# Kernel optimization log

Measured on AMD Instinct MI355X. Metric: run time of the kernel, lower is better.

The kernel has to match this reference:

```python
import jax, jax.numpy as jnp
import numpy as np

B, S, D, H = 4, 4096, 256, 4
Dh = D // H


def setup_inputs() -> dict:
    key = jax.random.key(0)
    ks = jax.random.split(key, 5)
    scale = 1.0 / np.sqrt(D)
    return {
        "inputs": jax.random.normal(ks[0], (B, S, D), dtype=jnp.float32),
        "Wq": jax.random.normal(ks[1], (D, D), dtype=jnp.float32) * scale,
        "bq": jnp.zeros((D,), jnp.float32),
        "Wk": jax.random.normal(ks[2], (D, D), dtype=jnp.float32) * scale,
        "bk": jnp.zeros((D,), jnp.float32),
        "Wv": jax.random.normal(ks[3], (D, D), dtype=jnp.float32) * scale,
        "bv": jnp.zeros((D,), jnp.float32),
        "Wo": jax.random.normal(ks[4], (D, D), dtype=jnp.float32) * scale,
        "bo": jnp.zeros((D,), jnp.float32),
    }


def reference(inputs, Wq, bq, Wk, bk, Wv, bv, Wo, bo):
    b, s, d = inputs.shape
    # QKV projections
    q = inputs @ Wq + bq
    k = inputs @ Wk + bk
    v = inputs @ Wv + bv
    # separate heads: [B, S, D] -> [B, H, S, Dh]
    def split_heads(x):
        return x.reshape(b, s, H, Dh).transpose(0, 2, 1, 3)
    q, k, v = split_heads(q), split_heads(k), split_heads(v)
    # scaled dot-product attention (no causal mask: mask=False)
    scores = jnp.einsum("bhqd,bhkd->bhqk", q, k) / jnp.sqrt(jnp.float32(Dh))
    weights = jax.nn.softmax(scores, axis=-1)
    attn = jnp.einsum("bhqk,bhkd->bhqd", weights, v)
    # combine heads: [B, H, S, Dh] -> [B, S, D]
    attn = attn.transpose(0, 2, 1, 3).reshape(b, s, d)
    return attn @ Wo + bo
```

## Files before the change

kernel.cpp:

```cpp
#include <hip/hip_runtime.h>
#include <cmath>

#define B_  4
#define S_  4096
#define D_  256
#define H_  4
#define DH_ 64
#define M_TOTAL (B_*S_)
#define QSCALE 0.1803368801111f

typedef __bf16 bf16x8 __attribute__((ext_vector_type(8)));
typedef __bf16 bf16x4 __attribute__((ext_vector_type(4)));
typedef __bf16 bf16x2 __attribute__((ext_vector_type(2)));
typedef float  f32x4  __attribute__((ext_vector_type(4)));
typedef float  f32x16 __attribute__((ext_vector_type(16)));

#define AS1 __attribute__((address_space(1)))
#define AS3 __attribute__((address_space(3)))

__device__ __forceinline__ void g2lds16(const void* g, void* l) {
    __builtin_amdgcn_global_load_lds((AS1 const void*)g, (AS3 void*)l, 16, 0, 0);
}

#if __has_builtin(__builtin_amdgcn_permlane32_swap)
typedef unsigned uint2v __attribute__((ext_vector_type(2)));
__device__ __forceinline__ void plswap(unsigned &a, unsigned &b) {
    uint2v r = __builtin_amdgcn_permlane32_swap(a, b, false, false);
    a = r[0]; b = r[1];
}
#else
__device__ __forceinline__ void plswap(unsigned &a, unsigned &b) {
    unsigned bl = (unsigned)__shfl_xor((int)b, 32);
    unsigned ah = (unsigned)__shfl_xor((int)a, 32);
    bool hi = (threadIdx.x & 32) != 0;
    unsigned na = hi ? bl : a;
    unsigned nb = hi ? b  : ah;
    a = na; b = nb;
}
#endif

__device__ __forceinline__ unsigned pk2(float x, float y) {
    bf16x2 t; t[0] = (__bf16)x; t[1] = (__bf16)y;
    return __builtin_bit_cast(unsigned, t);
}

__global__ __launch_bounds__(256) void prep(const float* __restrict__ X,
                                            const float* __restrict__ W0,
                                            const float* __restrict__ W1,
                                            const float* __restrict__ W2,
                                            const float* __restrict__ W3,
                                            __bf16* __restrict__ Xb,
                                            __bf16* __restrict__ Wt_all) {
    int t = threadIdx.x;
    if (blockIdx.x < 2048) {
        size_t i = ((size_t)blockIdx.x * 256 + t) * 8;
        float4 v0 = *(const float4*)(X + i);
        float4 v1 = *(const float4*)(X + i + 4);
        bf16x8 o;
        o[0] = (__bf16)v0.x; o[1] = (__bf16)v0.y; o[2] = (__bf16)v0.z; o[3] = (__bf16)v0.w;
        o[4] = (__bf16)v1.x; o[5] = (__bf16)v1.y; o[6] = (__bf16)v1.z; o[7] = (__bf16)v1.w;
        *(bf16x8*)(Xb + i) = o;
        return;
    }
    int bid = blockIdx.x - 2048;
    int z = bid >> 6, rem = bid & 63;
    int by = rem >> 3, bx = rem & 7;
    const float* W = (z == 0) ? W0 : (z == 1) ? W1 : (z == 2) ? W2 : W3;
    float wsc = (z == 0) ? QSCALE : 1.0f;
    __bf16* Wt = Wt_all + (size_t)z * 65536;
    __shared__ float tile[32][33];
    int r0 = by * 32, c0 = bx * 32;
#pragma unroll
    for (int e = 0; e < 4; e++) {
        int idx = t + e * 256; int r = idx >> 5, c = idx & 31;
        tile[r][c] = W[(r0 + r) * 256 + c0 + c];
    }
    __syncthreads();
#pragma unroll
    for (int e = 0; e < 4; e++) {
        int idx = t + e * 256; int r = idx >> 5, c = idx & 31;
        Wt[(c0 + r) * 256 + (r0 + c)] = (__bf16)(tile[c][r] * wsc);
    }
}

__global__ __launch_bounds__(256) void gemm_bt(const __bf16* __restrict__ A,
                                               const __bf16* __restrict__ Wt_all,
                                               const float* __restrict__ bias0,
                                               const float* __restrict__ bias1,
                                               const float* __restrict__ bias2,
                                               __bf16* __restrict__ outb,
                                               __bf16* __restrict__ voutb,
                                               float* __restrict__ outf,
                                               int out_is_f32, float bsc0) {
    constexpr int K = 256;
    __shared__ __attribute__((aligned(16))) __bf16 As[128 * 32];
    __shared__ __attribute__((aligned(16))) __bf16 Bs[128 * 32];

    int t = threadIdx.x;
    int lane = t & 63, w = t >> 6;
    int wr = w >> 1, wc = w & 1;
    int l16 = lane & 15, quad = lane >> 4;
    int mbase = blockIdx.x * 128;
    int nbase = blockIdx.y * 128;
    int z = blockIdx.z;
    const __bf16* Bt = Wt_all + (size_t)z * 65536;
    const float* bias = (z == 0) ? bias0 : (z == 1) ? bias1 : bias2;
    float bscale = (z == 0) ? bsc0 : 1.0f;

    f32x4 acc[4][4] = {};

    int srow = t >> 2;
    int sseg = (t & 3) * 8;

    for (int kk = 0; kk < K; kk += 32) {
        __syncthreads();
        g2lds16(A  + (size_t)(mbase +      srow) * K + kk + sseg, (char*)As +        t * 16);
        g2lds16(A  + (size_t)(mbase + 64 + srow) * K + kk + sseg, (char*)As + 4096 + t * 16);
        g2lds16(Bt + (size_t)(nbase +      srow) * K + kk + sseg, (char*)Bs +        t * 16);
        g2lds16(Bt + (size_t)(nbase + 64 + srow) * K + kk + sseg, (char*)Bs + 4096 + t * 16);
        __syncthreads();

        bf16x8 a[4], b[4];
#pragma unroll
        for (int i = 0; i < 4; i++)
            a[i] = *(const bf16x8*)(As + (wr * 64 + i * 16 + l16) * 32 + quad * 8);
#pragma unroll
        for (int j = 0; j < 4; j++)
            b[j] = *(const bf16x8*)(Bs + (wc * 64 + j * 16 + l16) * 32 + quad * 8);
#pragma unroll
        for (int i = 0; i < 4; i++)
#pragma unroll
            for (int j = 0; j < 4; j++)
                acc[i][j] = __builtin_amdgcn_mfma_f32_16x16x32_bf16(a[i], b[j], acc[i][j], 0, 0, 0);
    }

#pragma unroll
    for (int i = 0; i < 4; i++) {
#pragma unroll
        for (int j = 0; j < 4; j++) {
            int col = nbase + wc * 64 + j * 16 + l16;
            float bv = bias[col] * bscale;
            int row0 = mbase + wr * 64 + i * 16 + quad * 4;
            if (out_is_f32) {
#pragma unroll
                for (int r = 0; r < 4; r++)
                    outf[(size_t)(row0 + r) * 256 + col] = acc[i][j][r] + bv;
            } else if (z == 2) {
                int hcol = col >> 6, dh = col & 63;
                int bidx = row0 >> 12, s0 = row0 & 4095;
                bf16x4 pk;
#pragma unroll
                for (int r = 0; r < 4; r++) pk[r] = (__bf16)(acc[i][j][r] + bv);
                *(bf16x4*)(voutb + ((size_t)(bidx * 4 + hcol) * 64 + dh) * 4096 + s0) = pk;
            } else {
#pragma unroll
                for (int r = 0; r < 4; r++)
                    outb[(size_t)z * ((size_t)M_TOTAL * 256) + (size_t)(row0 + r) * 256 + col] =
                        (__bf16)(acc[i][j][r] + bv);
            }
        }
    }
}

__global__ __launch_bounds__(256, 2) void attn(const __bf16* __restrict__ Qb,
                                               const __bf16* __restrict__ Kb,
                                               const __bf16* __restrict__ Vt,
                                               __bf16* __restrict__ Ctx) {
    __shared__ __attribute__((aligned(16))) __bf16 smem[32768];

    int t = threadIdx.x;
    int lane = t & 63, w = t >> 6;
    int l31 = lane & 31, hh = lane >> 5;

    int lin = blockIdx.x;
    int xcd = lin & 7, j = lin >> 3;
    int bh = xcd * 2 + (j & 1);
    int qblk = j >> 1;
    int b = bh >> 2, hd = bh & 3;
    int qw = qblk * 128 + w * 32;

    const __bf16* Kbase = Kb + (size_t)b * S_ * 256 + hd * 64;
    const __bf16* Vbase = Vt + (size_t)bh * 64 * S_;

    bf16x8 qf[4];
#pragma unroll
    for (int ks = 0; ks < 4; ks++)
        qf[ks] = *(const bf16x8*)(Qb + (size_t)(b * S_ + qw + l31) * 256
                                      + hd * 64 + ks * 16 + hh * 8);

    f32x16 acc[2] = {};
    float lsum = 0.f;

    int srow = t >> 3;
    int sseg = t & 7;

#define STAGE(kv, slot) do {                                                   \
        char* mk = (char*)smem + (slot) * 16384;                               \
        char* mv = mk + 8192;                                                  \
        _Pragma("unroll")                                                      \
        for (int c = 0; c < 2; c++) {                                          \
            int rr = c * 32 + srow;                                            \
            int gseg = (sseg ^ (rr & 7)) * 8;                                  \
            g2lds16(Kbase + (size_t)((kv) + rr) * 256 + gseg,                  \
                    mk + c * 4096 + t * 16);                                   \
            g2lds16(Vbase + (size_t)rr * S_ + (kv) + gseg,                     \
                    mv + c * 4096 + t * 16);                                   \
        }                                                                      \
    } while (0)

    STAGE(0, 0);
    STAGE(64, 1);

    for (int it = 0; it < 64; it++) {
        if (it < 62) {
            STAGE((it + 2) * 64, (it + 2) & 3);
            asm volatile("s_waitcnt vmcnt(8)" ::: "memory");
        } else if (it == 62) {
            asm volatile("s_waitcnt vmcnt(4)" ::: "memory");
        } else {
            asm volatile("s_waitcnt vmcnt(0)" ::: "memory");
        }
        asm volatile("s_barrier" ::: "memory");

        __bf16* Ksp = (__bf16*)((char*)smem + (it & 3) * 16384);
        __bf16* Vsp = Ksp + 4096;

        f32x16 st[2] = {};
#pragma unroll
        for (int kt = 0; kt < 2; kt++) {
            bf16x8 kf[4];
#pragma unroll
            for (int ks = 0; ks < 4; ks++) {
                int slot = (ks * 2 + hh) ^ (l31 & 7);
                kf[ks] = *(const bf16x8*)(Ksp + (kt * 32 + l31) * 64 + slot * 8);
            }
#pragma unroll
            for (int ks = 0; ks < 4; ks++)
                st[kt] = __builtin_amdgcn_mfma_f32_32x32x16_bf16(kf[ks], qf[ks], st[kt], 0, 0, 0);
        }

#pragma unroll
        for (int kt = 0; kt < 2; kt++) {
            float p[16];
#pragma unroll
            for (int r = 0; r < 16; r++) p[r] = __builtin_amdgcn_exp2f(st[kt][r]);
            float s0 = ((p[0] + p[1]) + (p[2] + p[3])) + ((p[4] + p[5]) + (p[6] + p[7]));
            float s1 = ((p[8] + p[9]) + (p[10] + p[11])) + ((p[12] + p[13]) + (p[14] + p[15]));
            lsum += s0 + s1;
            unsigned dd[8];
#pragma unroll
            for (int m = 0; m < 4; m++) {
                dd[m * 2]     = pk2(p[4 * m],     p[4 * m + 1]);
                dd[m * 2 + 1] = pk2(p[4 * m + 2], p[4 * m + 3]);
            }
#pragma unroll
            for (int tt = 0; tt < 2; tt++) {
                int tks = kt * 2 + tt;
                unsigned x0 = dd[4 * tt],     y0 = dd[4 * tt + 2];
                unsigned x1 = dd[4 * tt + 1], y1 = dd[4 * tt + 3];
                plswap(x0, y0);
                plswap(x1, y1);
                union { unsigned u[4]; bf16x8 v; } c;
                c.u[0] = x0; c.u[1] = x1; c.u[2] = y0; c.u[3] = y1;
#pragma unroll
                for (int mt = 0; mt < 2; mt++) {
                    int slot = (tks * 2 + hh) ^ (l31 & 7);
                    bf16x8 vf = *(const bf16x8*)(Vsp + (mt * 32 + l31) * 64 + slot * 8);
                    acc[mt] = __builtin_amdgcn_mfma_f32_32x32x16_bf16(vf, c.v, acc[mt], 0, 0, 0);
                }
            }
        }
    }
#undef STAGE

    float l = lsum;
    l += __shfl_xor(l, 32);
    float inv = 1.f / l;

    __syncthreads();
    __bf16* Es = smem + w * 2304;
#pragma unroll
    for (int mt = 0; mt < 2; mt++) {
#pragma unroll
        for (int rg = 0; rg < 4; rg++) {
            bf16x4 ov;
#pragma unroll
            for (int e = 0; e < 4; e++) ov[e] = (__bf16)(acc[mt][4 * rg + e] * inv);
            int dhb = mt * 32 + rg * 8 + 4 * hh;
            *(bf16x4*)(Es + l31 * 72 + dhb) = ov;
        }
    }
    __syncthreads();
#pragma unroll
    for (int pass = 0; pass < 4; pass++) {
        int q = pass * 8 + (lane >> 3);
        int col = (lane & 7) * 8;
        bf16x8 val = *(const bf16x8*)(Es + q * 72 + col);
        *(bf16x8*)(Ctx + (size_t)(b * S_ + qw + q) * 256 + hd * 64 + col) = val;
    }
}

extern "C" void kernel_launch(void* const* d_in, const int* in_sizes, int n_in,
                              void* d_out, int out_size, void* d_ws, size_t ws_size,
                              hipStream_t stream) {
    const float* X  = (const float*)d_in[0];
    const float* Wq = (const float*)d_in[1];
    const float* bq = (const float*)d_in[2];
    const float* Wk = (const float*)d_in[3];
    const float* bk = (const float*)d_in[4];
    const float* Wv = (const float*)d_in[5];
    const float* bv = (const float*)d_in[6];
    const float* Wo = (const float*)d_in[7];
    const float* bo = (const float*)d_in[8];
    float* out = (float*)d_out;

    char* ws = (char*)d_ws;
    const size_t MB = 1024 * 1024;
    __bf16* Xb  = (__bf16*)(ws);
    __bf16* Ctx = (__bf16*)(ws);
    __bf16* Wt  = (__bf16*)(ws + 8 * MB);
    __bf16* Qb  = (__bf16*)(ws + 8 * MB + 512 * 1024);
    __bf16* Kb  = (__bf16*)((char*)Qb + 8 * MB);
    __bf16* Vt  = (__bf16*)((char*)Kb + 8 * MB);

    prep<<<dim3(2304), dim3(256), 0, stream>>>(X, Wq, Wk, Wv, Wo, Xb, Wt);
    gemm_bt<<<dim3(M_TOTAL / 128, 2, 3), dim3(256), 0, stream>>>(
        Xb, Wt, bq, bk, bv, Qb, Vt, nullptr, 0, QSCALE);
    attn<<<dim3(512), dim3(256), 0, stream>>>(Qb, Kb, Vt, Ctx);
    gemm_bt<<<dim3(M_TOTAL / 128, 2, 1), dim3(256), 0, stream>>>(
        Ctx, Wt + 3 * 65536, bo, bo, bo, nullptr, nullptr, out, 1, 1.0f);
}
```

Measured before the change: 181.6 us.

## Split attention KV tiles across warp pairs and load V directly to registers

```diff
diff --git a/kernel.cpp b/kernel.cpp
--- a/kernel.cpp
+++ b/kernel.cpp
@@ -162,22 +162,23 @@
     }
 }
 
-__global__ __launch_bounds__(256, 2) void attn(const __bf16* __restrict__ Qb,
+__global__ __launch_bounds__(256, 4) void attn(const __bf16* __restrict__ Qb,
                                                const __bf16* __restrict__ Kb,
                                                const __bf16* __restrict__ Vt,
                                                __bf16* __restrict__ Ctx) {
-    __shared__ __attribute__((aligned(16))) __bf16 smem[32768];
+    __shared__ __attribute__((aligned(16))) __bf16 smem[18432];
 
     int t = threadIdx.x;
     int lane = t & 63, w = t >> 6;
     int l31 = lane & 31, hh = lane >> 5;
+    int kw = w & 1, qw2 = w >> 1;
 
     int lin = blockIdx.x;
     int xcd = lin & 7, j = lin >> 3;
     int bh = xcd * 2 + (j & 1);
     int qblk = j >> 1;
     int b = bh >> 2, hd = bh & 3;
-    int qw = qblk * 128 + w * 32;
+    int qw = qblk * 64 + qw2 * 32;
 
     const __bf16* Kbase = Kb + (size_t)b * S_ * 256 + hd * 64;
     const __bf16* Vbase = Vt + (size_t)bh * 64 * S_;
@@ -195,16 +196,13 @@
     int sseg = t & 7;
 
 #define STAGE(kv, slot) do {                                                   \
-        char* mk = (char*)smem + (slot) * 16384;                               \
-        char* mv = mk + 8192;                                                  \
+        char* mk = (char*)smem + (slot) * 8192;                                \
         _Pragma("unroll")                                                      \
         for (int c = 0; c < 2; c++) {                                          \
             int rr = c * 32 + srow;                                            \
             int gseg = (sseg ^ (rr & 7)) * 8;                                  \
             g2lds16(Kbase + (size_t)((kv) + rr) * 256 + gseg,                  \
                     mk + c * 4096 + t * 16);                                   \
-            g2lds16(Vbase + (size_t)rr * S_ + (kv) + gseg,                     \
-                    mv + c * 4096 + t * 16);                                   \
         }                                                                      \
     } while (0)
 
@@ -212,91 +210,109 @@
     STAGE(64, 1);
 
     for (int it = 0; it < 64; it++) {
-        if (it < 62) {
-            STAGE((it + 2) * 64, (it + 2) & 3);
-            asm volatile("s_waitcnt vmcnt(8)" ::: "memory");
-        } else if (it == 62) {
-            asm volatile("s_waitcnt vmcnt(4)" ::: "memory");
-        } else {
-            asm volatile("s_waitcnt vmcnt(0)" ::: "memory");
-        }
+        int kv = it * 64;
+
+        bf16x8 vf[2][2];
+#pragma unroll
+        for (int tt = 0; tt < 2; tt++)
+#pragma unroll
+            for (int mt = 0; mt < 2; mt++)
+                vf[tt][mt] = *(const bf16x8*)(Vbase + (size_t)(mt * 32 + l31) * S_
+                                              + kv + (kw * 2 + tt) * 16 + hh * 8);
+
+        if (it < 62) STAGE(kv + 128, (it + 2) & 3);
+        asm volatile("s_waitcnt vmcnt(8)" ::: "memory");
         asm volatile("s_barrier" ::: "memory");
 
-        __bf16* Ksp = (__bf16*)((char*)smem + (it & 3) * 16384);
-        __bf16* Vsp = Ksp + 4096;
-
-        f32x16 st[2] = {};
-#pragma unroll
-        for (int kt = 0; kt < 2; kt++) {
-            bf16x8 kf[4];
-#pragma unroll
-            for (int ks = 0; ks < 4; ks++) {
-                int slot = (ks * 2 + hh) ^ (l31 & 7);
-                kf[ks] = *(const bf16x8*)(Ksp + (kt * 32 + l31) * 64 + slot * 8);
+        __bf16* Ksp = (__bf16*)((char*)smem + (it & 3) * 8192);
+
+        bf16x8 kf[4];
+#pragma unroll
+        for (int ks = 0; ks < 4; ks++) {
+            int slot = (ks * 2 + hh) ^ (l31 & 7);
+            kf[ks] = *(const bf16x8*)(Ksp + (kw * 32 + l31) * 64 + slot * 8);
+        }
+        f32x16 st = {};
+#pragma unroll
+        for (int ks = 0; ks < 4; ks++)
+            st = __builtin_amdgcn_mfma_f32_32x32x16_bf16(kf[ks], qf[ks], st, 0, 0, 0);
+
+        float p[16];
+#pragma unroll
+        for (int r = 0; r < 16; r++) p[r] = __builtin_amdgcn_exp2f(st[r]);
+        float s0 = ((p[0] + p[1]) + (p[2] + p[3])) + ((p[4] + p[5]) + (p[6] + p[7]));
+        float s1 = ((p[8] + p[9]) + (p[10] + p[11])) + ((p[12] + p[13]) + (p[14] + p[15]));
+        lsum += s0 + s1;
+        unsigned dd[8];
+#pragma unroll
+        for (int m = 0; m < 4; m++) {
+            dd[m * 2]     = pk2(p[4 * m],     p[4 * m + 1]);
+            dd[m * 2 + 1] = pk2(p[4 * m + 2], p[4 * m + 3]);
+        }
+
+#pragma unroll
+        for (int tt = 0; tt < 2; tt++) {
+            unsigned x0 = dd[4 * tt],     y0 = dd[4 * tt + 2];
+            unsigned x1 = dd[4 * tt + 1], y1 = dd[4 * tt + 3];
+            plswap(x0, y0);
+            plswap(x1, y1);
+            union { unsigned u[4]; bf16x8 v; } c;
+            c.u[0] = x0; c.u[1] = x1; c.u[2] = y0; c.u[3] = y1;
+#pragma unroll
+            for (int mt = 0; mt < 2; mt++)
+                acc[mt] = __builtin_amdgcn_mfma_f32_32x32x16_bf16(vf[tt][mt], c.v, acc[mt], 0, 0, 0);
+        }
+    }
+#undef STAGE
+
+    lsum += __shfl_xor(lsum, 32);
+
+    __syncthreads();
+    float* lsd = (float*)((char*)smem + 16384);
+    if (kw == 1) {
+#pragma unroll
+        for (int mt = 0; mt < 2; mt++)
+#pragma unroll
+            for (int g = 0; g < 4; g++) {
+                f32x4 v;
+#pragma unroll
+                for (int e = 0; e < 4; e++) v[e] = acc[mt][4 * g + e];
+                *(f32x4*)((char*)smem + qw2 * 8192 + (mt * 4 + g) * 1024 + lane * 16) = v;
             }
-#pragma unroll
-            for (int ks = 0; ks < 4; ks++)
-                st[kt] = __builtin_amdgcn_mfma_f32_32x32x16_bf16(kf[ks], qf[ks], st[kt], 0, 0, 0);
-        }
-
-#pragma unroll
-        for (int kt = 0; kt < 2; kt++) {
-            float p[16];
-#pragma unroll
-            for (int r = 0; r < 16; r++) p[r] = __builtin_amdgcn_exp2f(st[kt][r]);
-            float s0 = ((p[0] + p[1]) + (p[2] + p[3])) + ((p[4] + p[5]) + (p[6] + p[7]));
-            float s1 = ((p[8] + p[9]) + (p[10] + p[11])) + ((p[12] + p[13]) + (p[14] + p[15]));
-            lsum += s0 + s1;
-            unsigned dd[8];
-#pragma unroll
-            for (int m = 0; m < 4; m++) {
-                dd[m * 2]     = pk2(p[4 * m],     p[4 * m + 1]);
-                dd[m * 2 + 1] = pk2(p[4 * m + 2], p[4 * m + 3]);
+        lsd[qw2 * 64 + lane] = lsum;
+    }
+    __syncthreads();
+    if (kw == 0) {
+        float inv = 1.f / (lsum + lsd[qw2 * 64 + lane]);
+#pragma unroll
+        for (int mt = 0; mt < 2; mt++)
+#pragma unroll
+            for (int g = 0; g < 4; g++) {
+                f32x4 v = *(const f32x4*)((char*)smem + qw2 * 8192
+                                          + (mt * 4 + g) * 1024 + lane * 16);
+#pragma unroll
+                for (int e = 0; e < 4; e++) acc[mt][4 * g + e] += v[e];
             }
-#pragma unroll
-            for (int tt = 0; tt < 2; tt++) {
-                int tks = kt * 2 + tt;
-                unsigned x0 = dd[4 * tt],     y0 = dd[4 * tt + 2];
-                unsigned x1 = dd[4 * tt + 1], y1 = dd[4 * tt + 3];
-                plswap(x0, y0);
-                plswap(x1, y1);
-                union { unsigned u[4]; bf16x8 v; } c;
-                c.u[0] = x0; c.u[1] = x1; c.u[2] = y0; c.u[3] = y1;
-#pragma unroll
-                for (int mt = 0; mt < 2; mt++) {
-                    int slot = (tks * 2 + hh) ^ (l31 & 7);
-                    bf16x8 vf = *(const bf16x8*)(Vsp + (mt * 32 + l31) * 64 + slot * 8);
-                    acc[mt] = __builtin_amdgcn_mfma_f32_32x32x16_bf16(vf, c.v, acc[mt], 0, 0, 0);
-                }
+
+        __bf16* Es = (__bf16*)((char*)smem + 16896) + qw2 * 4608;
+#pragma unroll
+        for (int mt = 0; mt < 2; mt++)
+#pragma unroll
+            for (int rg = 0; rg < 4; rg++) {
+                bf16x4 ov;
+#pragma unroll
+                for (int e = 0; e < 4; e++)
+                    ov[e] = (__bf16)(acc[mt][4 * rg + e] * inv);
+                int dhb = mt * 32 + rg * 8 + 4 * hh;
+                *(bf16x4*)(Es + l31 * 72 + dhb) = ov;
             }
-        }
-    }
-#undef STAGE
-
-    float l = lsum;
-    l += __shfl_xor(l, 32);
-    float inv = 1.f / l;
-
-    __syncthreads();
-    __bf16* Es = smem + w * 2304;
-#pragma unroll
-    for (int mt = 0; mt < 2; mt++) {
-#pragma unroll
-        for (int rg = 0; rg < 4; rg++) {
-            bf16x4 ov;
-#pragma unroll
-            for (int e = 0; e < 4; e++) ov[e] = (__bf16)(acc[mt][4 * rg + e] * inv);
-            int dhb = mt * 32 + rg * 8 + 4 * hh;
-            *(bf16x4*)(Es + l31 * 72 + dhb) = ov;
-        }
-    }
-    __syncthreads();
-#pragma unroll
-    for (int pass = 0; pass < 4; pass++) {
-        int q = pass * 8 + (lane >> 3);
-        int col = (lane & 7) * 8;
-        bf16x8 val = *(const bf16x8*)(Es + q * 72 + col);
-        *(bf16x8*)(Ctx + (size_t)(b * S_ + qw + q) * 256 + hd * 64 + col) = val;
+#pragma unroll
+        for (int pass = 0; pass < 4; pass++) {
+            int q = pass * 8 + (lane >> 3);
+            int col = (lane & 7) * 8;
+            bf16x8 val = *(const bf16x8*)(Es + q * 72 + col);
+            *(bf16x8*)(Ctx + (size_t)(b * S_ + qw + q) * 256 + hd * 64 + col) = val;
+        }
     }
 }
 
@@ -326,7 +342,7 @@
     prep<<<dim3(2304), dim3(256), 0, stream>>>(X, Wq, Wk, Wv, Wo, Xb, Wt);
     gemm_bt<<<dim3(M_TOTAL / 128, 2, 3), dim3(256), 0, stream>>>(
         Xb, Wt, bq, bk, bv, Qb, Vt, nullptr, 0, QSCALE);
-    attn<<<dim3(512), dim3(256), 0, stream>>>(Qb, Kb, Vt, Ctx);
+    attn<<<dim3(1024), dim3(256), 0, stream>>>(Qb, Kb, Vt, Ctx);
     gemm_bt<<<dim3(M_TOTAL / 128, 2, 1), dim3(256), 0, stream>>>(
         Ctx, Wt + 3 * 65536, bo, bo, bo, nullptr, nullptr, out, 1, 1.0f);
 }
```

New measurement: 241.4 us. 1.33x slower.
